# Performance work log

Measured on AMD Instinct MI355X. Metric: run time of the kernel, lower is better.

## Reference

```python
import jax, jax.numpy as jnp
import numpy as np

N = 20000      # atoms
E = 320000     # edges
F = 128        # node_size (hard-pinned by split(128) / expand to 384)
RBF = 20
RC = 5.0
ITERS = 3
NM = 64        # molecules in batch


def setup_inputs() -> dict:
    key = jax.random.key(0)
    ks = iter(jax.random.split(key, 64))
    def nrm(shape, scale=0.05):
        return jax.random.normal(next(ks), shape, dtype=jnp.float32) * scale
    inp = {}
    inp["z"] = jax.random.randint(next(ks), (N,), 0, 119)
    inp["graph"] = jax.random.randint(next(ks), (E, 2), 0, N)
    inp["edges_dist"] = jax.random.uniform(next(ks), (E,), minval=0.5, maxval=RC, dtype=jnp.float32)
    sense = jax.random.normal(next(ks), (E, 3), dtype=jnp.float32)
    inp["edges_sense"] = sense / jnp.linalg.norm(sense, axis=1, keepdims=True)
    inp["graph_idx"] = jnp.sort(jax.random.randint(next(ks), (N,), 0, NM))
    # parameters (stacked over ITERS message/update blocks)
    inp["emb"] = nrm((119, F), 1.0)
    inp["mw1"] = nrm((ITERS, F, F)); inp["mb1"] = nrm((ITERS, F))
    inp["mw2"] = nrm((ITERS, 3 * F, F)); inp["mb2"] = nrm((ITERS, 3 * F))
    inp["ew"] = nrm((ITERS, 3 * F, RBF)); inp["eb"] = nrm((ITERS, 3 * F))
    inp["uw"] = nrm((ITERS, F, F)); inp["vw"] = nrm((ITERS, F, F))
    inp["aw1"] = nrm((ITERS, F, 2 * F)); inp["ab1"] = nrm((ITERS, F))
    inp["aw2"] = nrm((ITERS, 3 * F, F)); inp["ab2"] = nrm((ITERS, 3 * F))
    inp["ow1"] = nrm((F, F)); inp["ob1"] = nrm((F,))
    inp["ow2"] = nrm((1, F)); inp["ob2"] = nrm((1,))
    return inp


def reference(z, graph, edges_dist, edges_sense, graph_idx,
              emb, mw1, mb1, mw2, mb2, ew, eb,
              uw, vw, aw1, ab1, aw2, ab2, ow1, ob1, ow2, ob2):
    src = graph[:, 0]   # scatter target (index_add index)
    dst = graph[:, 1]   # gather source (neighbour)
    s = emb[z]                                  # [N, F]
    v = jnp.zeros((N, 3, F), dtype=s.dtype)     # [N, 3, F]
    # edge-level precompute (same every iteration)
    n = jnp.arange(1, RBF + 1, dtype=jnp.float32)
    d = edges_dist[:, None]
    rbf = jnp.sin(n * jnp.pi * d / RC) / d                              # [E, RBF]
    cut = 0.5 * (jnp.cos(jnp.pi * edges_dist / RC) + 1.0) * (edges_dist < RC)  # [E]
    for i in range(ITERS):
        # --- Message block ---
        a = jax.nn.silu(s @ mw1[i].T + mb1[i]) @ mw2[i].T + mb2[i]      # [N, 3F]
        dist_rep = (rbf @ ew[i].T + eb[i]) * cut[:, None]               # [E, 3F]
        res = a[dst] * dist_rep                                         # [E, 3F]
        rv, rs, rd = res[:, :F], res[:, F:2 * F], res[:, 2 * F:]
        resv = v[dst] * rv[:, None, :] + edges_sense[:, :, None] * rd[:, None, :]  # [E,3,F]
        s = s + 2.0 * jax.ops.segment_sum(rs, src, num_segments=N)
        v = v + 2.0 * jax.ops.segment_sum(resv, src, num_segments=N)
        # --- Update block ---
        Uv = v @ uw[i].T                                                # [N,3,F]
        Vv = v @ vw[i].T
        h = jnp.concatenate([s, jnp.linalg.norm(Vv, axis=1)], axis=-1)  # [N, 2F]
        a2 = jax.nn.silu(h @ aw1[i].T + ab1[i]) @ aw2[i].T + ab2[i]     # [N, 3F]
        avv, asv, ass = a2[:, :F], a2[:, F:2 * F], a2[:, 2 * F:]
        s = s + ass + asv * jnp.sum(Uv * Vv, axis=1)
        v = v + avv[:, None, :] * Uv
    out = jax.nn.silu(s @ ow1.T + ob1) @ ow2.T + ob2                    # [N, 1]
    return jax.ops.segment_sum(out, graph_idx, num_segments=NM)         # [NM, 1]
```

## Files before the change

kernel.cpp:

```cpp
#include <hip/hip_runtime.h>
#include <math.h>

#define NN 20000
#define NE 320000
#define FD 128
#define RBFN 20
#define RC_ 5.0f
#define NITER 3
#define NMOL 64
#define F3 384
#define F2 256
#define PI_ 3.14159265358979323846f
#define KB 128
#define LPAD 8
#define SDS 392

typedef __attribute__((ext_vector_type(8))) short  bf16x8;
typedef __attribute__((ext_vector_type(4))) float  floatx4;
typedef unsigned short u16;
typedef unsigned int   u32;

__device__ __forceinline__ u16 f2b(float x) {
    union { float f; unsigned int u; } v; v.f = x;
    unsigned int u = v.u;
    return (u16)((u + 0x7fffu + ((u >> 16) & 1u)) >> 16);
}
__device__ __forceinline__ float b2f(u16 x) {
    union { unsigned int u; float f; } v; v.u = ((unsigned int)x) << 16;
    return v.f;
}

__global__ __launch_bounds__(256) void cvt_w_kernel(
    const float* s0, int n0, const float* s1, int n1, const float* s2, int n2,
    const float* s3, int n3, const float* s4, int n4, const float* s5, int n5,
    const float* s6, int n6, u16* __restrict__ dst)
{
    int idx = blockIdx.x * 256 + threadIdx.x;
    if (idx < n0) { dst[idx] = f2b(s0[idx]); return; } idx -= n0; dst += n0;
    if (idx < n1) { dst[idx] = f2b(s1[idx]); return; } idx -= n1; dst += n1;
    if (idx < n2) { dst[idx] = f2b(s2[idx]); return; } idx -= n2; dst += n2;
    if (idx < n3) { dst[idx] = f2b(s3[idx]); return; } idx -= n3; dst += n3;
    if (idx < n4) { dst[idx] = f2b(s4[idx]); return; } idx -= n4; dst += n4;
    if (idx < n5) { dst[idx] = f2b(s5[idx]); return; } idx -= n5; dst += n5;
    if (idx < n6) { dst[idx] = f2b(s6[idx]); }
}

__global__ __launch_bounds__(256) void cvt_ew_kernel(const float* __restrict__ ew,
    u16* __restrict__ ewb)
{
    int idx = blockIdx.x * 256 + threadIdx.x;
    if (idx >= NITER * F3 * 32) return;
    int k = idx & 31;
    int row = idx >> 5;
    ewb[idx] = (k < RBFN) ? f2b(ew[row * RBFN + k]) : (u16)0;
}

__global__ __launch_bounds__(256) void embed_kernel(const int* __restrict__ z,
    const float* __restrict__ emb, float* __restrict__ s, u16* __restrict__ sbf)
{
    int idx = blockIdx.x * 256 + threadIdx.x;
    if (idx >= NN * FD) return;
    int n = idx >> 7, f = idx & 127;
    float v = emb[z[n] * FD + f];
    s[idx] = v; sbf[idx] = f2b(v);
}

__global__ __launch_bounds__(256) void zero_f_kernel(float* __restrict__ p, int n)
{
    int idx = blockIdx.x * 256 + threadIdx.x;
    if (idx < n) p[idx] = 0.f;
}

__global__ __launch_bounds__(256) void zero_i_kernel(int* __restrict__ p, int n)
{
    int idx = blockIdx.x * 256 + threadIdx.x;
    if (idx < n) p[idx] = 0;
}

__global__ __launch_bounds__(256) void csr_count_kernel(const int* __restrict__ graph,
    int* __restrict__ cnt)
{
    int e = blockIdx.x * 256 + threadIdx.x;
    if (e >= NE) return;
    atomicAdd(&cnt[graph[2 * e]], 1);
}

__global__ __launch_bounds__(1024) void csr_scan_kernel(const int* __restrict__ cnt,
    int* __restrict__ row_ptr, int* __restrict__ cursor)
{
    __shared__ int sd[1024];
    int tid = threadIdx.x;
    const int chunk = (NN + 1023) / 1024;
    int start = tid * chunk;
    int end = start + chunk; if (end > NN) end = NN;
    int sum = 0;
    for (int j = start; j < end; j++) sum += cnt[j];
    sd[tid] = sum;
    __syncthreads();
    for (int off = 1; off < 1024; off <<= 1) {
        int v = 0;
        if (tid >= off) v = sd[tid - off];
        __syncthreads();
        if (tid >= off) sd[tid] += v;
        __syncthreads();
    }
    int run = (tid == 0) ? 0 : sd[tid - 1];
    for (int j = start; j < end; j++) {
        row_ptr[j] = run;
        cursor[j]  = run;
        run += cnt[j];
    }
    if (tid == 0) row_ptr[NN] = NE;
}

__global__ __launch_bounds__(256) void csr_scatter_kernel(const int* __restrict__ graph,
    int* __restrict__ cursor, int* __restrict__ edge_list)
{
    int e = blockIdx.x * 256 + threadIdx.x;
    if (e >= NE) return;
    int p = atomicAdd(&cursor[graph[2 * e]], 1);
    edge_list[p] = e;
}

__global__ __launch_bounds__(256) void edge_stream_kernel(
    const int* __restrict__ edge_list, const int* __restrict__ graph,
    const float* __restrict__ dist, const float* __restrict__ sense,
    u16* __restrict__ rbf_bf, float* __restrict__ cut_p,
    float* __restrict__ sense_p, int* __restrict__ dst_p)
{
    int j = blockIdx.x * 256 + threadIdx.x;
    if (j >= NE) return;
    int e = edge_list[j];
    float d = dist[e];
    float inv = 1.f / d;
    float base = PI_ * d / RC_;
    u16* rb = rbf_bf + (size_t)j * 32;
    #pragma unroll
    for (int k = 0; k < RBFN; k++)
        rb[k] = f2b(sinf((float)(k + 1) * base) * inv);
    #pragma unroll
    for (int k = RBFN; k < 32; k++) rb[k] = 0;
    cut_p[j] = 0.5f * (cosf(base) + 1.f) * (d < RC_ ? 1.f : 0.f);
    dst_p[j] = graph[2 * e + 1];
    sense_p[3 * j + 0] = sense[3 * e + 0];
    sense_p[3 * j + 1] = sense[3 * e + 1];
    sense_p[3 * j + 2] = sense[3 * e + 2];
}

template<bool SILU>
__global__ __launch_bounds__(256) void gemm_bf16(const u16* __restrict__ A,
    const u16* __restrict__ Wt, const float* __restrict__ bias,
    float* __restrict__ C, int M, int K, int Nc)
{
    __shared__ u16 As[64][KB + LPAD];
    __shared__ u16 Bs[64][KB + LPAD];
    const int bm = blockIdx.x * 64;
    const int bn = blockIdx.y * 64;
    const int tid = threadIdx.x;
    const int r = tid >> 2;
    const int q = tid & 3;
    const int wave = tid >> 6;
    const int lane = tid & 63;
    const int wm = (wave >> 1) * 32;
    const int wn = (wave & 1) * 32;
    const int quad = lane >> 4;
    const int lr = lane & 15;

    floatx4 acc[2][2];
    #pragma unroll
    for (int i = 0; i < 2; i++)
        #pragma unroll
        for (int j = 0; j < 2; j++)
            acc[i][j] = (floatx4)0.f;

    for (int ko = 0; ko < K; ko += KB) {
        {
            int gm = bm + r;
            u16* dA = &As[r][q * 32];
            if (gm < M) {
                const u16* ap = A + (size_t)gm * K + ko + q * 32;
                #pragma unroll
                for (int x = 0; x < 32; x += 8)
                    *(bf16x8*)&dA[x] = *(const bf16x8*)(ap + x);
            } else {
                #pragma unroll
                for (int x = 0; x < 32; x += 8)
                    *(bf16x8*)&dA[x] = (bf16x8)0;
            }
        }
        {
            int gn = bn + r;
            const u16* wp = Wt + (size_t)gn * K + ko + q * 32;
            u16* dB = &Bs[r][q * 32];
            #pragma unroll
            for (int x = 0; x < 32; x += 8)
                *(bf16x8*)&dB[x] = *(const bf16x8*)(wp + x);
        }
        __syncthreads();
        #pragma unroll
        for (int kk = 0; kk < KB; kk += 32) {
            bf16x8 a0 = *(const bf16x8*)&As[wm + lr     ][kk + quad * 8];
            bf16x8 a1 = *(const bf16x8*)&As[wm + 16 + lr][kk + quad * 8];
            bf16x8 b0 = *(const bf16x8*)&Bs[wn + lr     ][kk + quad * 8];
            bf16x8 b1 = *(const bf16x8*)&Bs[wn + 16 + lr][kk + quad * 8];
            acc[0][0] = __builtin_amdgcn_mfma_f32_16x16x32_bf16(a0, b0, acc[0][0], 0, 0, 0);
            acc[0][1] = __builtin_amdgcn_mfma_f32_16x16x32_bf16(a0, b1, acc[0][1], 0, 0, 0);
            acc[1][0] = __builtin_amdgcn_mfma_f32_16x16x32_bf16(a1, b0, acc[1][0], 0, 0, 0);
            acc[1][1] = __builtin_amdgcn_mfma_f32_16x16x32_bf16(a1, b1, acc[1][1], 0, 0, 0);
        }
        __syncthreads();
    }

    #pragma unroll
    for (int i = 0; i < 2; i++) {
        #pragma unroll
        for (int j = 0; j < 2; j++) {
            int gn = bn + wn + j * 16 + lr;
            float bb = bias ? bias[gn] : 0.f;
            #pragma unroll
            for (int rr = 0; rr < 4; rr++) {
                int gm = bm + wm + i * 16 + quad * 4 + rr;
                if (gm < M) {
                    float v = acc[i][j][rr] + bb;
                    if (SILU) v = v / (1.f + __expf(-v));
                    C[(size_t)gm * Nc + gn] = v;
                }
            }
        }
    }
}

template<int K1, bool PACK>
__global__ __launch_bounds__(256) void mlp_kernel(const u16* __restrict__ A,
    const u16* __restrict__ W1, const float* __restrict__ b1,
    const u16* __restrict__ W2, const float* __restrict__ b2,
    u16* __restrict__ Ob, int M)
{
    __shared__ u16 As[64][KB + LPAD];
    __shared__ u16 Ws[128][KB + LPAD];
    __shared__ u16 T[64][KB + LPAD];
    const int bm = blockIdx.x * 64;
    const int tid = threadIdx.x;
    const int wave = tid >> 6, lane = tid & 63;
    const int wm  = (wave >> 1) * 32;
    const int wn1 = (wave & 1) * 64;
    const int wn  = (wave & 1) * 32;
    const int quad = lane >> 4, lr = lane & 15;
    const int r = tid >> 2, q = tid & 3;

    floatx4 acc1[2][4];
    #pragma unroll
    for (int i = 0; i < 2; i++)
        #pragma unroll
        for (int j = 0; j < 4; j++) acc1[i][j] = (floatx4)0.f;

    for (int ko = 0; ko < K1; ko += KB) {
        {
            int gm = bm + r;
            u16* dA = &As[r][q * 32];
            if (gm < M) {
                const u16* ap = A + (size_t)gm * K1 + ko + q * 32;
                #pragma unroll
                for (int x = 0; x < 32; x += 8)
                    *(bf16x8*)&dA[x] = *(const bf16x8*)(ap + x);
            } else {
                #pragma unroll
                for (int x = 0; x < 32; x += 8)
                    *(bf16x8*)&dA[x] = (bf16x8)0;
            }
            #pragma unroll
            for (int h = 0; h < 2; h++) {
                int wr = r + h * 64;
                const u16* wp = W1 + (size_t)wr * K1 + ko + q * 32;
                u16* dW = &Ws[wr][q * 32];
                #pragma unroll
                for (int x = 0; x < 32; x += 8)
                    *(bf16x8*)&dW[x] = *(const bf16x8*)(wp + x);
            }
        }
        __syncthreads();
        #pragma unroll
        for (int kk = 0; kk < KB; kk += 32) {
            bf16x8 a0 = *(const bf16x8*)&As[wm + lr     ][kk + quad * 8];
            bf16x8 a1 = *(const bf16x8*)&As[wm + 16 + lr][kk + quad * 8];
            #pragma unroll
            for (int j = 0; j < 4; j++) {
                bf16x8 b = *(const bf16x8*)&Ws[wn1 + j * 16 + lr][kk + quad * 8];
                acc1[0][j] = __builtin_amdgcn_mfma_f32_16x16x32_bf16(a0, b, acc1[0][j], 0, 0, 0);
                acc1[1][j] = __builtin_amdgcn_mfma_f32_16x16x32_bf16(a1, b, acc1[1][j], 0, 0, 0);
            }
        }
        __syncthreads();
    }
    #pragma unroll
    for (int i = 0; i < 2; i++) {
        #pragma unroll
        for (int j = 0; j < 4; j++) {
            int col = wn1 + j * 16 + lr;
            float bb = b1[col];
            #pragma unroll
            for (int rr = 0; rr < 4; rr++) {
                int row = wm + i * 16 + quad * 4 + rr;
                float v = acc1[i][j][rr] + bb;
                v = v / (1.f + __expf(-v));
                T[row][col] = f2b(v);
            }
        }
    }
    __syncthreads();

    for (int c0 = 0; c0 < F3; c0 += 64) {
        {
            const u16* wp = W2 + (size_t)(c0 + r) * KB + q * 32;
            u16* dW = &Ws[r][q * 32];
            #pragma unroll
            for (int x = 0; x < 32; x += 8)
                *(bf16x8*)&dW[x] = *(const bf16x8*)(wp + x);
        }
        __syncthreads();
        floatx4 acc2[2][2];
        #pragma unroll
        for (int i = 0; i < 2; i++)
            #pragma unroll
            for (int j = 0; j < 2; j++) acc2[i][j] = (floatx4)0.f;
        #pragma unroll
        for (int kk = 0; kk < KB; kk += 32) {
            bf16x8 a0 = *(const bf16x8*)&T[wm + lr     ][kk + quad * 8];
            bf16x8 a1 = *(const bf16x8*)&T[wm + 16 + lr][kk + quad * 8];
            bf16x8 b0 = *(const bf16x8*)&Ws[wn + lr     ][kk + quad * 8];
            bf16x8 b1 = *(const bf16x8*)&Ws[wn + 16 + lr][kk + quad * 8];
            acc2[0][0] = __builtin_amdgcn_mfma_f32_16x16x32_bf16(a0, b0, acc2[0][0], 0, 0, 0);
            acc2[0][1] = __builtin_amdgcn_mfma_f32_16x16x32_bf16(a0, b1, acc2[0][1], 0, 0, 0);
            acc2[1][0] = __builtin_amdgcn_mfma_f32_16x16x32_bf16(a1, b0, acc2[1][0], 0, 0, 0);
            acc2[1][1] = __builtin_amdgcn_mfma_f32_16x16x32_bf16(a1, b1, acc2[1][1], 0, 0, 0);
        }
        #pragma unroll
        for (int i = 0; i < 2; i++) {
            #pragma unroll
            for (int j = 0; j < 2; j++) {
                int gn = c0 + wn + j * 16 + lr;
                float bb = b2[gn];
                #pragma unroll
                for (int rr = 0; rr < 4; rr++) {
                    int gm = bm + wm + i * 16 + quad * 4 + rr;
                    if (gm < M) {
                        u16 val = f2b(acc2[i][j][rr] + bb);
                        if (PACK) {
                            int off = (gn < 256) ? ((gn & 127) * 2 + (gn >> 7))
                                                 : (256 + (gn & 127));
                            Ob[(size_t)gm * F3 + off] = val;
                        } else {
                            Ob[(size_t)gm * F3 + gn] = val;
                        }
                    }
                }
            }
        }
        __syncthreads();
    }
}

__global__ __launch_bounds__(256) void gemm_uv(const u16* __restrict__ A,
    const u16* __restrict__ Wu, const u16* __restrict__ Wv,
    u16* __restrict__ U, u16* __restrict__ V, int M)
{
    __shared__ u16 As[64][KB + LPAD];
    __shared__ u16 Bu[64][KB + LPAD];
    __shared__ u16 Bv[64][KB + LPAD];
    const int bm = blockIdx.x * 64;
    const int bn = blockIdx.y * 64;
    const int tid = threadIdx.x;
    const int r = tid >> 2;
    const int q = tid & 3;
    const int wave = tid >> 6;
    const int lane = tid & 63;
    const int wm = (wave >> 1) * 32;
    const int wn = (wave & 1) * 32;
    const int quad = lane >> 4;
    const int lr = lane & 15;

    floatx4 au[2][2], av[2][2];
    #pragma unroll
    for (int i = 0; i < 2; i++)
        #pragma unroll
        for (int j = 0; j < 2; j++) { au[i][j] = (floatx4)0.f; av[i][j] = (floatx4)0.f; }

    {
        int gm = bm + r;
        u16* dA = &As[r][q * 32];
        if (gm < M) {
            const u16* ap = A + (size_t)gm * KB + q * 32;
            #pragma unroll
            for (int x = 0; x < 32; x += 8)
                *(bf16x8*)&dA[x] = *(const bf16x8*)(ap + x);
        } else {
            #pragma unroll
            for (int x = 0; x < 32; x += 8)
                *(bf16x8*)&dA[x] = (bf16x8)0;
        }
        int gn = bn + r;
        const u16* up = Wu + (size_t)gn * KB + q * 32;
        const u16* vp = Wv + (size_t)gn * KB + q * 32;
        u16* dU = &Bu[r][q * 32];
        u16* dV = &Bv[r][q * 32];
        #pragma unroll
        for (int x = 0; x < 32; x += 8) {
            *(bf16x8*)&dU[x] = *(const bf16x8*)(up + x);
            *(bf16x8*)&dV[x] = *(const bf16x8*)(vp + x);
        }
    }
    __syncthreads();
    #pragma unroll
    for (int kk = 0; kk < KB; kk += 32) {
        bf16x8 a0 = *(const bf16x8*)&As[wm + lr     ][kk + quad * 8];
        bf16x8 a1 = *(const bf16x8*)&As[wm + 16 + lr][kk + quad * 8];
        bf16x8 u0 = *(const bf16x8*)&Bu[wn + lr     ][kk + quad * 8];
        bf16x8 u1 = *(const bf16x8*)&Bu[wn + 16 + lr][kk + quad * 8];
        bf16x8 v0 = *(const bf16x8*)&Bv[wn + lr     ][kk + quad * 8];
        bf16x8 v1 = *(const bf16x8*)&Bv[wn + 16 + lr][kk + quad * 8];
        au[0][0] = __builtin_amdgcn_mfma_f32_16x16x32_bf16(a0, u0, au[0][0], 0, 0, 0);
        au[0][1] = __builtin_amdgcn_mfma_f32_16x16x32_bf16(a0, u1, au[0][1], 0, 0, 0);
        au[1][0] = __builtin_amdgcn_mfma_f32_16x16x32_bf16(a1, u0, au[1][0], 0, 0, 0);
        au[1][1] = __builtin_amdgcn_mfma_f32_16x16x32_bf16(a1, u1, au[1][1], 0, 0, 0);
        av[0][0] = __builtin_amdgcn_mfma_f32_16x16x32_bf16(a0, v0, av[0][0], 0, 0, 0);
        av[0][1] = __builtin_amdgcn_mfma_f32_16x16x32_bf16(a0, v1, av[0][1], 0, 0, 0);
        av[1][0] = __builtin_amdgcn_mfma_f32_16x16x32_bf16(a1, v0, av[1][0], 0, 0, 0);
        av[1][1] = __builtin_amdgcn_mfma_f32_16x16x32_bf16(a1, v1, av[1][1], 0, 0, 0);
    }
    #pragma unroll
    for (int i = 0; i < 2; i++) {
        #pragma unroll
        for (int j = 0; j < 2; j++) {
            int gn = bn + wn + j * 16 + lr;
            #pragma unroll
            for (int rr = 0; rr < 4; rr++) {
                int gm = bm + wm + i * 16 + quad * 4 + rr;
                if (gm < M) {
                    U[(size_t)gm * FD + gn] = f2b(au[i][j][rr]);
                    V[(size_t)gm * FD + gn] = f2b(av[i][j][rr]);
                }
            }
        }
    }
}

__global__ __launch_bounds__(256) void edge_mfma_kernel(
    const u16* __restrict__ rbf_bf, const float* __restrict__ cut_p,
    const float* __restrict__ sense_p, const int* __restrict__ dst_p,
    const u16* __restrict__ ewb, const float* __restrict__ eb,
    const u16* __restrict__ a_pk, const float* __restrict__ s_in,
    const float* __restrict__ v_in, const u16* __restrict__ v_pk,
    const int* __restrict__ row_ptr,
    float* __restrict__ s_out, u16* __restrict__ s_obf,
    float* __restrict__ v_out, u16* __restrict__ v_obf)
{
    __shared__ u16   sdrep[16 * SDS];
    __shared__ float scut[16];
    __shared__ float ssen[16][4];
    __shared__ int   sdst[16];
    __shared__ float red[4 * 128];

    const int n = blockIdx.x;
    const int tid = threadIdx.x;
    const int wave = tid >> 6;
    const int lane = tid & 63;
    const int quad = lane >> 4;
    const int lr = lane & 15;
    const int f = tid & 127;
    const int half = tid >> 7;

    int beg = row_ptr[n], end = row_ptr[n + 1];
    float accs = 0.f, accv0 = 0.f, accv1 = 0.f, accv2 = 0.f;

    for (int t0 = beg; t0 < end; t0 += 16) {
        int cnt = end - t0; if (cnt > 16) cnt = 16;
        __syncthreads();
        if (tid < 16) {
            scut[tid] = (tid < cnt) ? cut_p[t0 + tid] : 0.f;
            sdst[tid] = (tid < cnt) ? dst_p[t0 + tid] : 0;
        }
        if (tid >= 64 && tid < 64 + 3 * cnt) {
            int x = tid - 64;
            ssen[x / 3][x % 3] = sense_p[3 * t0 + x];
        }
        bf16x8 afrag;
        int ge = t0 + lr;
        if (ge < end) afrag = *(const bf16x8*)&rbf_bf[(size_t)ge * 32 + quad * 8];
        else          afrag = (bf16x8)0;
        floatx4 dacc[6];
        #pragma unroll
        for (int nt = 0; nt < 6; nt++) {
            int nrow = (wave * 6 + nt) * 16 + lr;
            bf16x8 bfrag = *(const bf16x8*)&ewb[(size_t)nrow * 32 + quad * 8];
            dacc[nt] = __builtin_amdgcn_mfma_f32_16x16x32_bf16(afrag, bfrag, (floatx4)0.f, 0, 0, 0);
        }
        __syncthreads();
        #pragma unroll
        for (int nt = 0; nt < 6; nt++) {
            int ncol = (wave * 6 + nt) * 16 + lr;
            float ebn = eb[ncol];
            #pragma unroll
            for (int rr = 0; rr < 4; rr++) {
                int e = quad * 4 + rr;
                sdrep[e * SDS + ncol] = f2b((dacc[nt][rr] + ebn) * scut[e]);
            }
        }
        __syncthreads();
        int nh = cnt - half * 8; if (nh > 8) nh = 8;
        for (int k = 0; k < nh; k++) {
            int e = half * 8 + k;
            int dst = sdst[e];
            const u16* sr = &sdrep[e * SDS];
            float drv = b2f(sr[f]);
            float drs = b2f(sr[FD + f]);
            float drd = b2f(sr[2 * FD + f]);
            const u16* ar = a_pk + (size_t)dst * F3;
            u32 ap = *(const u32*)(ar + f * 2);
            float rv = b2f((u16)(ap & 0xffff)) * drv;
            float rs = b2f((u16)(ap >> 16))    * drs;
            float rd = b2f(ar[256 + f])        * drd;
            accs += rs;
            const u16* vr = v_pk + (size_t)dst * F3;
            u32 vp = *(const u32*)(vr + f * 2);
            accv0 += b2f((u16)(vp & 0xffff)) * rv + ssen[e][0] * rd;
            accv1 += b2f((u16)(vp >> 16))    * rv + ssen[e][1] * rd;
            accv2 += b2f(vr[256 + f])        * rv + ssen[e][2] * rd;
        }
    }
    __syncthreads();
    if (half == 1) {
        red[f] = accs; red[128 + f] = accv0; red[256 + f] = accv1; red[384 + f] = accv2;
    }
    __syncthreads();
    if (half == 0) {
        accs  += red[f];       accv0 += red[128 + f];
        accv1 += red[256 + f]; accv2 += red[384 + f];
        int nb = n * FD + f;
        float so = s_in[nb] + 2.f * accs;
        s_out[nb] = so; s_obf[nb] = f2b(so);
        int vb = n * F3 + f;
        float w0 = v_in[vb]           + 2.f * accv0;
        float w1 = v_in[vb + FD]      + 2.f * accv1;
        float w2 = v_in[vb + 2 * FD]  + 2.f * accv2;
        v_out[vb]          = w0; v_obf[vb]          = f2b(w0);
        v_out[vb + FD]     = w1; v_obf[vb + FD]     = f2b(w1);
        v_out[vb + 2 * FD] = w2; v_obf[vb + 2 * FD] = f2b(w2);
    }
}

__global__ __launch_bounds__(256) void build_h_kernel(const u16* __restrict__ sbf,
    const u16* __restrict__ Vv, u16* __restrict__ h)
{
    int idx = blockIdx.x * 256 + threadIdx.x;
    if (idx >= NN * FD) return;
    int n = idx >> 7, f = idx & 127;
    h[n * F2 + f] = sbf[idx];
    float x0 = b2f(Vv[n * F3 + f]);
    float x1 = b2f(Vv[n * F3 + FD + f]);
    float x2 = b2f(Vv[n * F3 + 2 * FD + f]);
    h[n * F2 + FD + f] = f2b(sqrtf(x0 * x0 + x1 * x1 + x2 * x2));
}

__global__ __launch_bounds__(256) void update_kernel(const float* __restrict__ s_mid,
    const float* __restrict__ v_mid, const u16* __restrict__ a2,
    const u16* __restrict__ Uv, const u16* __restrict__ Vv,
    float* __restrict__ s_out, u16* __restrict__ s_obf,
    float* __restrict__ v_out, u16* __restrict__ v_pk)
{
    int idx = blockIdx.x * 256 + threadIdx.x;
    if (idx >= NN * FD) return;
    int n = idx >> 7, f = idx & 127;
    int vb = n * F3 + f;
    float u0 = b2f(Uv[vb]), u1 = b2f(Uv[vb + FD]), u2 = b2f(Uv[vb + 2 * FD]);
    float w0 = b2f(Vv[vb]), w1 = b2f(Vv[vb + FD]), w2 = b2f(Vv[vb + 2 * FD]);
    float dot = u0 * w0 + u1 * w1 + u2 * w2;
    float avv = b2f(a2[n * F3 + f]);
    float asv = b2f(a2[n * F3 + FD + f]);
    float ass = b2f(a2[n * F3 + 2 * FD + f]);
    float so = s_mid[idx] + ass + asv * dot;
    s_out[idx] = so; s_obf[idx] = f2b(so);
    float y0 = v_mid[vb]          + avv * u0;
    float y1 = v_mid[vb + FD]     + avv * u1;
    float y2 = v_mid[vb + 2 * FD] + avv * u2;
    v_out[vb]          = y0;
    v_out[vb + FD]     = y1;
    v_out[vb + 2 * FD] = y2;
    u16* vp = v_pk + (size_t)n * F3;
    *(u32*)(vp + f * 2) = (u32)f2b(y0) | ((u32)f2b(y1) << 16);
    vp[256 + f] = f2b(y2);
}

__global__ __launch_bounds__(256) void node_out_kernel(const float* __restrict__ t,
    const float* __restrict__ ow2, const float* __restrict__ ob2,
    float* __restrict__ nodeval)
{
    int gt = blockIdx.x * 256 + threadIdx.x;
    int n = gt >> 6;
    int lane = threadIdx.x & 63;
    if (n >= NN) return;
    float v = t[n * FD + lane] * ow2[lane] + t[n * FD + 64 + lane] * ow2[64 + lane];
    #pragma unroll
    for (int off = 32; off > 0; off >>= 1) v += __shfl_down(v, off);
    if (lane == 0) nodeval[n] = v + ob2[0];
}

__global__ __launch_bounds__(1024) void mol_reduce_kernel(const float* __restrict__ nodeval,
    const int* __restrict__ gidx, float* __restrict__ out)
{
    __shared__ float mol[NMOL];
    int tid = threadIdx.x;
    if (tid < NMOL) mol[tid] = 0.f;
    __syncthreads();
    int cur = -1; float acc = 0.f;
    for (int x = tid; x < NN; x += 1024) {
        int g = gidx[x];
        float v = nodeval[x];
        if (g != cur) {
            if (cur >= 0) atomicAdd(&mol[cur], acc);
            cur = g; acc = v;
        } else acc += v;
    }
    if (cur >= 0) atomicAdd(&mol[cur], acc);
    __syncthreads();
    if (tid < NMOL) out[tid] = mol[tid];
}

extern "C" void kernel_launch(void* const* d_in, const int* in_sizes, int n_in,
                              void* d_out, int out_size, void* d_ws, size_t ws_size,
                              hipStream_t stream)
{
    const int*   z     = (const int*)d_in[0];
    const int*   graph = (const int*)d_in[1];
    const float* dist  = (const float*)d_in[2];
    const float* sense = (const float*)d_in[3];
    const int*   gidx  = (const int*)d_in[4];
    const float* emb   = (const float*)d_in[5];
    const float* mw1   = (const float*)d_in[6];
    const float* mb1   = (const float*)d_in[7];
    const float* mw2   = (const float*)d_in[8];
    const float* mb2   = (const float*)d_in[9];
    const float* ew    = (const float*)d_in[10];
    const float* eb    = (const float*)d_in[11];
    const float* uw    = (const float*)d_in[12];
    const float* vw    = (const float*)d_in[13];
    const float* aw1   = (const float*)d_in[14];
    const float* ab1   = (const float*)d_in[15];
    const float* aw2   = (const float*)d_in[16];
    const float* ab2   = (const float*)d_in[17];
    const float* ow1   = (const float*)d_in[18];
    const float* ob1   = (const float*)d_in[19];
    const float* ow2   = (const float*)d_in[20];
    const float* ob2   = (const float*)d_in[21];
    float* out = (float*)d_out;

    float* W = (float*)d_ws;
    float* s_a    = W; W += (size_t)NN * FD;
    float* s_b    = W; W += (size_t)NN * FD;
    float* v_a    = W; W += (size_t)NN * F3;
    float* v_b    = W; W += (size_t)NN * F3;
    float* cut_p  = W; W += (size_t)NE;
    float* sns_p  = W; W += (size_t)NE * 3;
    float* nodeval= W; W += (size_t)NN;
    u16* U = (u16*)W;
    u16* sbf_a = U; U += (size_t)NN * FD;
    u16* sbf_b = U; U += (size_t)NN * FD;
    u16* vbf_b = U; U += (size_t)NN * F3;
    u16* a_pk  = U; U += (size_t)NN * F3;
    u16* v_pk  = U; U += (size_t)NN * F3;
    u16* h_bf  = U; U += (size_t)NN * F2;
    u16* a2_bf = U; U += (size_t)NN * F3;
    u16* Uv_bf = U; U += (size_t)NN * F3;
    u16* Vv_bf = U; U += (size_t)NN * F3;
    u16* rbf_bf= U; U += (size_t)NE * 32;
    u16* ewb   = U; U += (size_t)NITER * F3 * 32;
    u16* wb    = U; U += 557056;
    int* ip = (int*)U;
    int* row_ptr   = ip; ip += NN + 1;
    int* cnt       = ip; ip += NN;
    int* cursor    = ip; ip += NN;
    int* edge_list = ip; ip += NE;
    int* dst_p     = ip; ip += NE;
    float* tfin = s_b;

    u16* wb_mw1 = wb;
    u16* wb_mw2 = wb + 49152;
    u16* wb_uw  = wb + 196608;
    u16* wb_vw  = wb + 245760;
    u16* wb_aw1 = wb + 294912;
    u16* wb_aw2 = wb + 393216;
    u16* wb_ow1 = wb + 540672;
    const int WTOT = 557056;

    const int TB = 256;
    dim3 b256(TB);

    cvt_w_kernel<<<dim3((WTOT + TB - 1) / TB), b256, 0, stream>>>(
        mw1, 49152, mw2, 147456, uw, 49152, vw, 49152, aw1, 98304, aw2, 147456,
        ow1, 16384, wb);
    cvt_ew_kernel<<<dim3((NITER * F3 * 32 + TB - 1) / TB), b256, 0, stream>>>(ew, ewb);
    embed_kernel<<<dim3((NN * FD + TB - 1) / TB), b256, 0, stream>>>(z, emb, s_a, sbf_a);
    zero_f_kernel<<<dim3((NN * F3 + TB - 1) / TB), b256, 0, stream>>>(v_a, NN * F3);
    zero_i_kernel<<<dim3((NN * F3 / 2 + TB - 1) / TB), b256, 0, stream>>>((int*)v_pk, NN * F3 / 2);
    zero_i_kernel<<<dim3((NN + TB - 1) / TB), b256, 0, stream>>>(cnt, NN);
    csr_count_kernel<<<dim3((NE + TB - 1) / TB), b256, 0, stream>>>(graph, cnt);
    csr_scan_kernel<<<dim3(1), dim3(1024), 0, stream>>>(cnt, row_ptr, cursor);
    csr_scatter_kernel<<<dim3((NE + TB - 1) / TB), b256, 0, stream>>>(graph, cursor, edge_list);
    edge_stream_kernel<<<dim3((NE + TB - 1) / TB), b256, 0, stream>>>(
        edge_list, graph, dist, sense, rbf_bf, cut_p, sns_p, dst_p);

    dim3 gM((NN + 63) / 64);
    dim3 gN2((NN + 63) / 64, FD / 64);
    dim3 gV2((3 * NN + 63) / 64, FD / 64);

    for (int i = 0; i < NITER; i++) {
        mlp_kernel<128, true><<<gM, b256, 0, stream>>>(sbf_a,
            wb_mw1 + (size_t)i * FD * FD, mb1 + (size_t)i * FD,
            wb_mw2 + (size_t)i * F3 * FD, mb2 + (size_t)i * F3, a_pk, NN);
        edge_mfma_kernel<<<dim3(NN), b256, 0, stream>>>(
            rbf_bf, cut_p, sns_p, dst_p,
            ewb + (size_t)i * F3 * 32, eb + (size_t)i * F3,
            a_pk, s_a, v_a, v_pk, row_ptr, s_b, sbf_b, v_b, vbf_b);
        gemm_uv<<<gV2, b256, 0, stream>>>(vbf_b, wb_uw + (size_t)i * FD * FD,
            wb_vw + (size_t)i * FD * FD, Uv_bf, Vv_bf, 3 * NN);
        build_h_kernel<<<dim3((NN * FD + TB - 1) / TB), b256, 0, stream>>>(sbf_b, Vv_bf, h_bf);
        mlp_kernel<256, false><<<gM, b256, 0, stream>>>(h_bf,
            wb_aw1 + (size_t)i * FD * F2, ab1 + (size_t)i * FD,
            wb_aw2 + (size_t)i * F3 * FD, ab2 + (size_t)i * F3, a2_bf, NN);
        update_kernel<<<dim3((NN * FD + TB - 1) / TB), b256, 0, stream>>>(
            s_b, v_b, a2_bf, Uv_bf, Vv_bf, s_a, sbf_a, v_a, v_pk);
    }

    gemm_bf16<true><<<gN2, b256, 0, stream>>>(sbf_a, wb_ow1, ob1, tfin, NN, FD, FD);
    node_out_kernel<<<dim3((NN * 64 + TB - 1) / TB), b256, 0, stream>>>(tfin, ow2, ob2, nodeval);
    mol_reduce_kernel<<<dim3(1), dim3(1024), 0, stream>>>(nodeval, gidx, out);
}
```

Measured before the change: 948.9 us.

## Interleave message and vector features per node for wider gathers in edge kernel

The separate packed message buffer and packed vector buffer are merged into one per-node 768-element interleaved row, so each edge reads a (rv, rs, v0, v1) quad with one 8-byte load and a (rd, v2) pair with one 4-byte load, where it used to issue several scattered loads across two buffers. The MLP epilogue and the update kernel now write into this shared layout, and the edge-filter LDS tile is stored in a matching packed order so each edge needs two LDS reads instead of three. The edge-filter weight fragments and bias are also hoisted into registers once per block rather than reloaded every 16-edge tile. The merge adds register pressure and makes the producers write strided, interleaved rows.

```diff
diff --git a/kernel.cpp b/kernel.cpp
--- a/kernel.cpp
+++ b/kernel.cpp
@@ -346,9 +346,9 @@
                     if (gm < M) {
                         u16 val = f2b(acc2[i][j][rr] + bb);
                         if (PACK) {
-                            int off = (gn < 256) ? ((gn & 127) * 2 + (gn >> 7))
-                                                 : (256 + (gn & 127));
-                            Ob[(size_t)gm * F3 + off] = val;
+                            int fc = gn & 127;
+                            int off = (gn < 256) ? (fc * 4 + (gn >> 7)) : (512 + fc * 2);
+                            Ob[(size_t)gm * 768 + off] = val;
                         } else {
                             Ob[(size_t)gm * F3 + gn] = val;
                         }
@@ -448,8 +448,8 @@
     const u16* __restrict__ rbf_bf, const float* __restrict__ cut_p,
     const float* __restrict__ sense_p, const int* __restrict__ dst_p,
     const u16* __restrict__ ewb, const float* __restrict__ eb,
-    const u16* __restrict__ a_pk, const float* __restrict__ s_in,
-    const float* __restrict__ v_in, const u16* __restrict__ v_pk,
+    const u16* __restrict__ apv, const float* __restrict__ s_in,
+    const float* __restrict__ v_in,
     const int* __restrict__ row_ptr,
     float* __restrict__ s_out, u16* __restrict__ s_obf,
     float* __restrict__ v_out, u16* __restrict__ v_obf)
@@ -469,6 +469,15 @@
     const int f = tid & 127;
     const int half = tid >> 7;
 
+    bf16x8 bfrag[6];
+    float  ebv[6];
+    #pragma unroll
+    for (int nt = 0; nt < 6; nt++) {
+        int nrow = (wave * 6 + nt) * 16 + lr;
+        bfrag[nt] = *(const bf16x8*)&ewb[(size_t)nrow * 32 + quad * 8];
+        ebv[nt]   = eb[nrow];
+    }
+
     int beg = row_ptr[n], end = row_ptr[n + 1];
     float accs = 0.f, accv0 = 0.f, accv1 = 0.f, accv2 = 0.f;
 
@@ -489,42 +498,40 @@
         else          afrag = (bf16x8)0;
         floatx4 dacc[6];
         #pragma unroll
-        for (int nt = 0; nt < 6; nt++) {
-            int nrow = (wave * 6 + nt) * 16 + lr;
-            bf16x8 bfrag = *(const bf16x8*)&ewb[(size_t)nrow * 32 + quad * 8];
-            dacc[nt] = __builtin_amdgcn_mfma_f32_16x16x32_bf16(afrag, bfrag, (floatx4)0.f, 0, 0, 0);
-        }
+        for (int nt = 0; nt < 6; nt++)
+            dacc[nt] = __builtin_amdgcn_mfma_f32_16x16x32_bf16(afrag, bfrag[nt], (floatx4)0.f, 0, 0, 0);
         __syncthreads();
         #pragma unroll
         for (int nt = 0; nt < 6; nt++) {
             int ncol = (wave * 6 + nt) * 16 + lr;
-            float ebn = eb[ncol];
+            int fc = ncol & 127;
+            int off = (ncol < 256) ? (fc * 2 + (ncol >> 7)) : (256 + fc);
             #pragma unroll
             for (int rr = 0; rr < 4; rr++) {
                 int e = quad * 4 + rr;
-                sdrep[e * SDS + ncol] = f2b((dacc[nt][rr] + ebn) * scut[e]);
+                sdrep[e * SDS + off] = f2b((dacc[nt][rr] + ebv[nt]) * scut[e]);
             }
         }
         __syncthreads();
         int nh = cnt - half * 8; if (nh > 8) nh = 8;
+        int base = half * 8;
         for (int k = 0; k < nh; k++) {
-            int e = half * 8 + k;
+            int e = base + k;
             int dst = sdst[e];
-            const u16* sr = &sdrep[e * SDS];
-            float drv = b2f(sr[f]);
-            float drs = b2f(sr[FD + f]);
-            float drd = b2f(sr[2 * FD + f]);
-            const u16* ar = a_pk + (size_t)dst * F3;
-            u32 ap = *(const u32*)(ar + f * 2);
-            float rv = b2f((u16)(ap & 0xffff)) * drv;
-            float rs = b2f((u16)(ap >> 16))    * drs;
-            float rd = b2f(ar[256 + f])        * drd;
+            u32 drp = *(const u32*)&sdrep[e * SDS + f * 2];
+            float drv = b2f((u16)(drp & 0xffff));
+            float drs = b2f((u16)(drp >> 16));
+            float drd = b2f(sdrep[e * SDS + 256 + f]);
+            const u16* row = apv + (size_t)dst * 768;
+            uint2 qv = *(const uint2*)(row + f * 4);
+            u32  p2 = *(const u32*)(row + 512 + f * 2);
+            float rv = b2f((u16)(qv.x & 0xffff)) * drv;
+            float rs = b2f((u16)(qv.x >> 16))    * drs;
+            float rd = b2f((u16)(p2 & 0xffff))   * drd;
             accs += rs;
-            const u16* vr = v_pk + (size_t)dst * F3;
-            u32 vp = *(const u32*)(vr + f * 2);
-            accv0 += b2f((u16)(vp & 0xffff)) * rv + ssen[e][0] * rd;
-            accv1 += b2f((u16)(vp >> 16))    * rv + ssen[e][1] * rd;
-            accv2 += b2f(vr[256 + f])        * rv + ssen[e][2] * rd;
+            accv0 += b2f((u16)(qv.y & 0xffff)) * rv + ssen[e][0] * rd;
+            accv1 += b2f((u16)(qv.y >> 16))    * rv + ssen[e][1] * rd;
+            accv2 += b2f((u16)(p2 >> 16))      * rv + ssen[e][2] * rd;
         }
     }
     __syncthreads();
@@ -565,7 +572,7 @@
     const float* __restrict__ v_mid, const u16* __restrict__ a2,
     const u16* __restrict__ Uv, const u16* __restrict__ Vv,
     float* __restrict__ s_out, u16* __restrict__ s_obf,
-    float* __restrict__ v_out, u16* __restrict__ v_pk)
+    float* __restrict__ v_out, u16* __restrict__ apv)
 {
     int idx = blockIdx.x * 256 + threadIdx.x;
     if (idx >= NN * FD) return;
@@ -585,9 +592,9 @@
     v_out[vb]          = y0;
     v_out[vb + FD]     = y1;
     v_out[vb + 2 * FD] = y2;
-    u16* vp = v_pk + (size_t)n * F3;
-    *(u32*)(vp + f * 2) = (u32)f2b(y0) | ((u32)f2b(y1) << 16);
-    vp[256 + f] = f2b(y2);
+    u16* vp = apv + (size_t)n * 768;
+    *(u32*)(vp + f * 4 + 2) = (u32)f2b(y0) | ((u32)f2b(y1) << 16);
+    vp[512 + f * 2 + 1] = f2b(y2);
 }
 
 __global__ __launch_bounds__(256) void node_out_kernel(const float* __restrict__ t,
@@ -665,8 +672,7 @@
     u16* sbf_a = U; U += (size_t)NN * FD;
     u16* sbf_b = U; U += (size_t)NN * FD;
     u16* vbf_b = U; U += (size_t)NN * F3;
-    u16* a_pk  = U; U += (size_t)NN * F3;
-    u16* v_pk  = U; U += (size_t)NN * F3;
+    u16* apv   = U; U += (size_t)NN * 768;
     u16* h_bf  = U; U += (size_t)NN * F2;
     u16* a2_bf = U; U += (size_t)NN * F3;
     u16* Uv_bf = U; U += (size_t)NN * F3;
@@ -700,7 +706,7 @@
     cvt_ew_kernel<<<dim3((NITER * F3 * 32 + TB - 1) / TB), b256, 0, stream>>>(ew, ewb);
     embed_kernel<<<dim3((NN * FD + TB - 1) / TB), b256, 0, stream>>>(z, emb, s_a, sbf_a);
     zero_f_kernel<<<dim3((NN * F3 + TB - 1) / TB), b256, 0, stream>>>(v_a, NN * F3);
-    zero_i_kernel<<<dim3((NN * F3 / 2 + TB - 1) / TB), b256, 0, stream>>>((int*)v_pk, NN * F3 / 2);
+    zero_i_kernel<<<dim3((NN * 384 + TB - 1) / TB), b256, 0, stream>>>((int*)apv, NN * 384);
     zero_i_kernel<<<dim3((NN + TB - 1) / TB), b256, 0, stream>>>(cnt, NN);
     csr_count_kernel<<<dim3((NE + TB - 1) / TB), b256, 0, stream>>>(graph, cnt);
     csr_scan_kernel<<<dim3(1), dim3(1024), 0, stream>>>(cnt, row_ptr, cursor);
@@ -715,11 +721,11 @@
     for (int i = 0; i < NITER; i++) {
         mlp_kernel<128, true><<<gM, b256, 0, stream>>>(sbf_a,
             wb_mw1 + (size_t)i * FD * FD, mb1 + (size_t)i * FD,
-            wb_mw2 + (size_t)i * F3 * FD, mb2 + (size_t)i * F3, a_pk, NN);
+            wb_mw2 + (size_t)i * F3 * FD, mb2 + (size_t)i * F3, apv, NN);
         edge_mfma_kernel<<<dim3(NN), b256, 0, stream>>>(
             rbf_bf, cut_p, sns_p, dst_p,
             ewb + (size_t)i * F3 * 32, eb + (size_t)i * F3,
-            a_pk, s_a, v_a, v_pk, row_ptr, s_b, sbf_b, v_b, vbf_b);
+            apv, s_a, v_a, row_ptr, s_b, sbf_b, v_b, vbf_b);
         gemm_uv<<<gV2, b256, 0, stream>>>(vbf_b, wb_uw + (size_t)i * FD * FD,
             wb_vw + (size_t)i * FD * FD, Uv_bf, Vv_bf, 3 * NN);
         build_h_kernel<<<dim3((NN * FD + TB - 1) / TB), b256, 0, stream>>>(sbf_b, Vv_bf, h_bf);
@@ -727,7 +733,7 @@
             wb_aw1 + (size_t)i * FD * F2, ab1 + (size_t)i * FD,
             wb_aw2 + (size_t)i * F3 * FD, ab2 + (size_t)i * F3, a2_bf, NN);
         update_kernel<<<dim3((NN * FD + TB - 1) / TB), b256, 0, stream>>>(
-            s_b, v_b, a2_bf, Uv_bf, Vv_bf, s_a, sbf_a, v_a, v_pk);
+            s_b, v_b, a2_bf, Uv_bf, Vv_bf, s_a, sbf_a, v_a, apv);
     }
 
     gemm_bf16<true><<<gN2, b256, 0, stream>>>(sbf_a, wb_ow1, ob1, tfin, NN, FD, FD);
```

New measurement: 988.9 us. 1.04x slower.

## Widen edge kernel to 512 threads, hoist edge weights, pack dist_rep in LDS

Applied to the files above, without the earlier changes.

The per-node edge kernel now runs 512 threads (8 waves), so each wave computes 3 MFMA column tiles instead of 6. The edge-weight fragments and biases are loaded once into registers before the edge loop instead of being reloaded for every 16-edge chunk. The dist_rep tile in shared memory is stored in the same interleaved layout as a_pk, so v/s pairs are read with one 32-bit load. The four thread groups each handle 4 of the 16 edges in a chunk and are reduced through a larger shared buffer. This adds parallelism for the gather-heavy loop, at the cost of idle threads on low-degree nodes and extra reduction work.

```diff
diff --git a/kernel.cpp b/kernel.cpp
--- a/kernel.cpp
+++ b/kernel.cpp
@@ -346,8 +346,8 @@
                     if (gm < M) {
                         u16 val = f2b(acc2[i][j][rr] + bb);
                         if (PACK) {
-                            int off = (gn < 256) ? ((gn & 127) * 2 + (gn >> 7))
-                                                 : (256 + (gn & 127));
+                            int fc = gn & 127;
+                            int off = (gn < 256) ? (fc * 2 + (gn >> 7)) : (256 + fc);
                             Ob[(size_t)gm * F3 + off] = val;
                         } else {
                             Ob[(size_t)gm * F3 + gn] = val;
@@ -444,7 +444,7 @@
     }
 }
 
-__global__ __launch_bounds__(256) void edge_mfma_kernel(
+__global__ __launch_bounds__(512) void edge_mfma_kernel(
     const u16* __restrict__ rbf_bf, const float* __restrict__ cut_p,
     const float* __restrict__ sense_p, const int* __restrict__ dst_p,
     const u16* __restrict__ ewb, const float* __restrict__ eb,
@@ -458,7 +458,7 @@
     __shared__ float scut[16];
     __shared__ float ssen[16][4];
     __shared__ int   sdst[16];
-    __shared__ float red[4 * 128];
+    __shared__ float red[3 * 512];
 
     const int n = blockIdx.x;
     const int tid = threadIdx.x;
@@ -467,7 +467,16 @@
     const int quad = lane >> 4;
     const int lr = lane & 15;
     const int f = tid & 127;
-    const int half = tid >> 7;
+    const int qt = tid >> 7;
+
+    bf16x8 bfrag[3];
+    float  ebv[3];
+    #pragma unroll
+    for (int nt = 0; nt < 3; nt++) {
+        int nrow = (wave * 3 + nt) * 16 + lr;
+        bfrag[nt] = *(const bf16x8*)&ewb[(size_t)nrow * 32 + quad * 8];
+        ebv[nt]   = eb[nrow];
+    }
 
     int beg = row_ptr[n], end = row_ptr[n + 1];
     float accs = 0.f, accv0 = 0.f, accv1 = 0.f, accv2 = 0.f;
@@ -487,33 +496,32 @@
         int ge = t0 + lr;
         if (ge < end) afrag = *(const bf16x8*)&rbf_bf[(size_t)ge * 32 + quad * 8];
         else          afrag = (bf16x8)0;
-        floatx4 dacc[6];
-        #pragma unroll
-        for (int nt = 0; nt < 6; nt++) {
-            int nrow = (wave * 6 + nt) * 16 + lr;
-            bf16x8 bfrag = *(const bf16x8*)&ewb[(size_t)nrow * 32 + quad * 8];
-            dacc[nt] = __builtin_amdgcn_mfma_f32_16x16x32_bf16(afrag, bfrag, (floatx4)0.f, 0, 0, 0);
-        }
-        __syncthreads();
-        #pragma unroll
-        for (int nt = 0; nt < 6; nt++) {
-            int ncol = (wave * 6 + nt) * 16 + lr;
-            float ebn = eb[ncol];
+        floatx4 dacc[3];
+        #pragma unroll
+        for (int nt = 0; nt < 3; nt++)
+            dacc[nt] = __builtin_amdgcn_mfma_f32_16x16x32_bf16(afrag, bfrag[nt], (floatx4)0.f, 0, 0, 0);
+        __syncthreads();
+        #pragma unroll
+        for (int nt = 0; nt < 3; nt++) {
+            int ncol = (wave * 3 + nt) * 16 + lr;
+            int fc = ncol & 127;
+            int off = (ncol < 256) ? (fc * 2 + (ncol >> 7)) : (256 + fc);
             #pragma unroll
             for (int rr = 0; rr < 4; rr++) {
                 int e = quad * 4 + rr;
-                sdrep[e * SDS + ncol] = f2b((dacc[nt][rr] + ebn) * scut[e]);
-            }
-        }
-        __syncthreads();
-        int nh = cnt - half * 8; if (nh > 8) nh = 8;
+                sdrep[e * SDS + off] = f2b((dacc[nt][rr] + ebv[nt]) * scut[e]);
+            }
+        }
+        __syncthreads();
+        int base = qt * 4;
+        int nh = cnt - base; if (nh > 4) nh = 4;
         for (int k = 0; k < nh; k++) {
-            int e = half * 8 + k;
+            int e = base + k;
             int dst = sdst[e];
-            const u16* sr = &sdrep[e * SDS];
-            float drv = b2f(sr[f]);
-            float drs = b2f(sr[FD + f]);
-            float drd = b2f(sr[2 * FD + f]);
+            u32 drp = *(const u32*)&sdrep[e * SDS + f * 2];
+            float drv = b2f((u16)(drp & 0xffff));
+            float drs = b2f((u16)(drp >> 16));
+            float drd = b2f(sdrep[e * SDS + 256 + f]);
             const u16* ar = a_pk + (size_t)dst * F3;
             u32 ap = *(const u32*)(ar + f * 2);
             float rv = b2f((u16)(ap & 0xffff)) * drv;
@@ -528,13 +536,18 @@
         }
     }
     __syncthreads();
-    if (half == 1) {
-        red[f] = accs; red[128 + f] = accv0; red[256 + f] = accv1; red[384 + f] = accv2;
+    if (qt > 0) {
+        float* rp = &red[(qt - 1) * 512];
+        rp[f] = accs; rp[128 + f] = accv0; rp[256 + f] = accv1; rp[384 + f] = accv2;
     }
     __syncthreads();
-    if (half == 0) {
-        accs  += red[f];       accv0 += red[128 + f];
-        accv1 += red[256 + f]; accv2 += red[384 + f];
+    if (qt == 0) {
+        #pragma unroll
+        for (int qq = 0; qq < 3; qq++) {
+            const float* rp = &red[qq * 512];
+            accs  += rp[f];       accv0 += rp[128 + f];
+            accv1 += rp[256 + f]; accv2 += rp[384 + f];
+        }
         int nb = n * FD + f;
         float so = s_in[nb] + 2.f * accs;
         s_out[nb] = so; s_obf[nb] = f2b(so);
@@ -716,7 +729,7 @@
         mlp_kernel<128, true><<<gM, b256, 0, stream>>>(sbf_a,
             wb_mw1 + (size_t)i * FD * FD, mb1 + (size_t)i * FD,
             wb_mw2 + (size_t)i * F3 * FD, mb2 + (size_t)i * F3, a_pk, NN);
-        edge_mfma_kernel<<<dim3(NN), b256, 0, stream>>>(
+        edge_mfma_kernel<<<dim3(NN), dim3(512), 0, stream>>>(
             rbf_bf, cut_p, sns_p, dst_p,
             ewb + (size_t)i * F3 * 32, eb + (size_t)i * F3,
             a_pk, s_a, v_a, v_pk, row_ptr, s_b, sbf_b, v_b, vbf_b);
```

Result: slower. 1.034 ms (+8.9%).

## Fuse vector-norm h construction into update MLP and hoist edge weight fragments

Applied to the files above, without the earlier changes.

Replaces the separate build_h kernel and the generic two-layer MLP with a dedicated kernel that builds the [s, |Vv|] input tile directly in shared memory while loading, removing the intermediate h buffer write and read plus one launch. The edge kernel now loads its RBF weight fragments and biases into registers once per block instead of every 16-edge tile. It also stores the dist_rep tile in the interleaved packed layout so the v/s components are read with one 32-bit LDS load. This adds register pressure in the edge kernel and recomputes the norm per M-tile, which is not redundant here since each N tile covers all columns.

```diff
diff --git a/kernel.cpp b/kernel.cpp
--- a/kernel.cpp
+++ b/kernel.cpp
@@ -346,13 +346,154 @@
                     if (gm < M) {
                         u16 val = f2b(acc2[i][j][rr] + bb);
                         if (PACK) {
-                            int off = (gn < 256) ? ((gn & 127) * 2 + (gn >> 7))
-                                                 : (256 + (gn & 127));
+                            int fc = gn & 127;
+                            int off = (gn < 256) ? (fc * 2 + (gn >> 7)) : (256 + fc);
                             Ob[(size_t)gm * F3 + off] = val;
                         } else {
                             Ob[(size_t)gm * F3 + gn] = val;
                         }
                     }
+                }
+            }
+        }
+        __syncthreads();
+    }
+}
+
+__global__ __launch_bounds__(256) void amlp_kernel(const u16* __restrict__ sbf,
+    const u16* __restrict__ Vv,
+    const u16* __restrict__ W1, const float* __restrict__ b1,
+    const u16* __restrict__ W2, const float* __restrict__ b2,
+    u16* __restrict__ Ob, int M)
+{
+    __shared__ u16 As[64][KB + LPAD];
+    __shared__ u16 Ws[128][KB + LPAD];
+    __shared__ u16 T[64][KB + LPAD];
+    const int bm = blockIdx.x * 64;
+    const int tid = threadIdx.x;
+    const int wave = tid >> 6, lane = tid & 63;
+    const int wm  = (wave >> 1) * 32;
+    const int wn1 = (wave & 1) * 64;
+    const int wn  = (wave & 1) * 32;
+    const int quad = lane >> 4, lr = lane & 15;
+    const int r = tid >> 2, q = tid & 3;
+
+    floatx4 acc1[2][4];
+    #pragma unroll
+    for (int i = 0; i < 2; i++)
+        #pragma unroll
+        for (int j = 0; j < 4; j++) acc1[i][j] = (floatx4)0.f;
+
+    for (int ko = 0; ko < F2; ko += KB) {
+        {
+            int gm = bm + r;
+            u16* dA = &As[r][q * 32];
+            if (gm < M) {
+                if (ko == 0) {
+                    const u16* ap = sbf + (size_t)gm * FD + q * 32;
+                    #pragma unroll
+                    for (int x = 0; x < 32; x += 8)
+                        *(bf16x8*)&dA[x] = *(const bf16x8*)(ap + x);
+                } else {
+                    const u16* vr = Vv + (size_t)gm * F3 + q * 32;
+                    #pragma unroll
+                    for (int x = 0; x < 32; x += 8) {
+                        bf16x8 c0 = *(const bf16x8*)(vr + x);
+                        bf16x8 c1 = *(const bf16x8*)(vr + FD + x);
+                        bf16x8 c2 = *(const bf16x8*)(vr + 2 * FD + x);
+                        bf16x8 o;
+                        #pragma unroll
+                        for (int t = 0; t < 8; t++) {
+                            float a = b2f((u16)c0[t]);
+                            float b = b2f((u16)c1[t]);
+                            float c = b2f((u16)c2[t]);
+                            o[t] = (short)f2b(sqrtf(a * a + b * b + c * c));
+                        }
+                        *(bf16x8*)&dA[x] = o;
+                    }
+                }
+            } else {
+                #pragma unroll
+                for (int x = 0; x < 32; x += 8)
+                    *(bf16x8*)&dA[x] = (bf16x8)0;
+            }
+            #pragma unroll
+            for (int h = 0; h < 2; h++) {
+                int wr = r + h * 64;
+                const u16* wp = W1 + (size_t)wr * F2 + ko + q * 32;
+                u16* dW = &Ws[wr][q * 32];
+                #pragma unroll
+                for (int x = 0; x < 32; x += 8)
+                    *(bf16x8*)&dW[x] = *(const bf16x8*)(wp + x);
+            }
+        }
+        __syncthreads();
+        #pragma unroll
+        for (int kk = 0; kk < KB; kk += 32) {
+            bf16x8 a0 = *(const bf16x8*)&As[wm + lr     ][kk + quad * 8];
+            bf16x8 a1 = *(const bf16x8*)&As[wm + 16 + lr][kk + quad * 8];
+            #pragma unroll
+            for (int j = 0; j < 4; j++) {
+                bf16x8 b = *(const bf16x8*)&Ws[wn1 + j * 16 + lr][kk + quad * 8];
+                acc1[0][j] = __builtin_amdgcn_mfma_f32_16x16x32_bf16(a0, b, acc1[0][j], 0, 0, 0);
+                acc1[1][j] = __builtin_amdgcn_mfma_f32_16x16x32_bf16(a1, b, acc1[1][j], 0, 0, 0);
+            }
+        }
+        __syncthreads();
+    }
+    #pragma unroll
+    for (int i = 0; i < 2; i++) {
+        #pragma unroll
+        for (int j = 0; j < 4; j++) {
+            int col = wn1 + j * 16 + lr;
+            float bb = b1[col];
+            #pragma unroll
+            for (int rr = 0; rr < 4; rr++) {
+                int row = wm + i * 16 + quad * 4 + rr;
+                float v = acc1[i][j][rr] + bb;
+                v = v / (1.f + __expf(-v));
+                T[row][col] = f2b(v);
+            }
+        }
+    }
+    __syncthreads();
+
+    for (int c0 = 0; c0 < F3; c0 += 64) {
+        {
+            const u16* wp = W2 + (size_t)(c0 + r) * KB + q * 32;
+            u16* dW = &Ws[r][q * 32];
+            #pragma unroll
+            for (int x = 0; x < 32; x += 8)
+                *(bf16x8*)&dW[x] = *(const bf16x8*)(wp + x);
+        }
+        __syncthreads();
+        floatx4 acc2[2][2];
+        #pragma unroll
+        for (int i = 0; i < 2; i++)
+            #pragma unroll
+            for (int j = 0; j < 2; j++) acc2[i][j] = (floatx4)0.f;
+        #pragma unroll
+        for (int kk = 0; kk < KB; kk += 32) {
+            bf16x8 a0 = *(const bf16x8*)&T[wm + lr     ][kk + quad * 8];
+            bf16x8 a1 = *(const bf16x8*)&T[wm + 16 + lr][kk + quad * 8];
+            bf16x8 b0 = *(const bf16x8*)&Ws[wn + lr     ][kk + quad * 8];
+            bf16x8 b1 = *(const bf16x8*)&Ws[wn + 16 + lr][kk + quad * 8];
+            acc2[0][0] = __builtin_amdgcn_mfma_f32_16x16x32_bf16(a0, b0, acc2[0][0], 0, 0, 0);
+            acc2[0][1] = __builtin_amdgcn_mfma_f32_16x16x32_bf16(a0, b1, acc2[0][1], 0, 0, 0);
+            acc2[1][0] = __builtin_amdgcn_mfma_f32_16x16x32_bf16(a1, b0, acc2[1][0], 0, 0, 0);
+            acc2[1][1] = __builtin_amdgcn_mfma_f32_16x16x32_bf16(a1, b1, acc2[1][1], 0, 0, 0);
+        }
+        #pragma unroll
+        for (int i = 0; i < 2; i++) {
+            #pragma unroll
+            for (int j = 0; j < 2; j++) {
+                int gn = c0 + wn + j * 16 + lr;
+                float bb = b2[gn];
+                #pragma unroll
+                for (int rr = 0; rr < 4; rr++) {
+                    int gm = bm + wm + i * 16 + quad * 4 + rr;
+                    if (gm < M)
+                        Ob[(size_t)gm * F3 + gn] = f2b(acc2[i][j][rr] + bb);
                 }
             }
         }
@@ -469,6 +610,15 @@
     const int f = tid & 127;
     const int half = tid >> 7;
 
+    bf16x8 bfrag[6];
+    float  ebv[6];
+    #pragma unroll
+    for (int nt = 0; nt < 6; nt++) {
+        int nrow = (wave * 6 + nt) * 16 + lr;
+        bfrag[nt] = *(const bf16x8*)&ewb[(size_t)nrow * 32 + quad * 8];
+        ebv[nt]   = eb[nrow];
+    }
+
     int beg = row_ptr[n], end = row_ptr[n + 1];
     float accs = 0.f, accv0 = 0.f, accv1 = 0.f, accv2 = 0.f;
 
@@ -489,31 +639,30 @@
         else          afrag = (bf16x8)0;
         floatx4 dacc[6];
         #pragma unroll
-        for (int nt = 0; nt < 6; nt++) {
-            int nrow = (wave * 6 + nt) * 16 + lr;
-            bf16x8 bfrag = *(const bf16x8*)&ewb[(size_t)nrow * 32 + quad * 8];
-            dacc[nt] = __builtin_amdgcn_mfma_f32_16x16x32_bf16(afrag, bfrag, (floatx4)0.f, 0, 0, 0);
-        }
+        for (int nt = 0; nt < 6; nt++)
+            dacc[nt] = __builtin_amdgcn_mfma_f32_16x16x32_bf16(afrag, bfrag[nt], (floatx4)0.f, 0, 0, 0);
         __syncthreads();
         #pragma unroll
         for (int nt = 0; nt < 6; nt++) {
             int ncol = (wave * 6 + nt) * 16 + lr;
-            float ebn = eb[ncol];
+            int fc = ncol & 127;
+            int off = (ncol < 256) ? (fc * 2 + (ncol >> 7)) : (256 + fc);
             #pragma unroll
             for (int rr = 0; rr < 4; rr++) {
                 int e = quad * 4 + rr;
-                sdrep[e * SDS + ncol] = f2b((dacc[nt][rr] + ebn) * scut[e]);
+                sdrep[e * SDS + off] = f2b((dacc[nt][rr] + ebv[nt]) * scut[e]);
             }
         }
         __syncthreads();
         int nh = cnt - half * 8; if (nh > 8) nh = 8;
+        int base = half * 8;
         for (int k = 0; k < nh; k++) {
-            int e = half * 8 + k;
+            int e = base + k;
             int dst = sdst[e];
-            const u16* sr = &sdrep[e * SDS];
-            float drv = b2f(sr[f]);
-            float drs = b2f(sr[FD + f]);
-            float drd = b2f(sr[2 * FD + f]);
+            u32 drp = *(const u32*)&sdrep[e * SDS + f * 2];
+            float drv = b2f((u16)(drp & 0xffff));
+            float drs = b2f((u16)(drp >> 16));
+            float drd = b2f(sdrep[e * SDS + 256 + f]);
             const u16* ar = a_pk + (size_t)dst * F3;
             u32 ap = *(const u32*)(ar + f * 2);
             float rv = b2f((u16)(ap & 0xffff)) * drv;
@@ -546,19 +695,6 @@
         v_out[vb + FD]     = w1; v_obf[vb + FD]     = f2b(w1);
         v_out[vb + 2 * FD] = w2; v_obf[vb + 2 * FD] = f2b(w2);
     }
-}
-
-__global__ __launch_bounds__(256) void build_h_kernel(const u16* __restrict__ sbf,
-    const u16* __restrict__ Vv, u16* __restrict__ h)
-{
-    int idx = blockIdx.x * 256 + threadIdx.x;
-    if (idx >= NN * FD) return;
-    int n = idx >> 7, f = idx & 127;
-    h[n * F2 + f] = sbf[idx];
-    float x0 = b2f(Vv[n * F3 + f]);
-    float x1 = b2f(Vv[n * F3 + FD + f]);
-    float x2 = b2f(Vv[n * F3 + 2 * FD + f]);
-    h[n * F2 + FD + f] = f2b(sqrtf(x0 * x0 + x1 * x1 + x2 * x2));
 }
 
 __global__ __launch_bounds__(256) void update_kernel(const float* __restrict__ s_mid,
@@ -667,7 +803,6 @@
     u16* vbf_b = U; U += (size_t)NN * F3;
     u16* a_pk  = U; U += (size_t)NN * F3;
     u16* v_pk  = U; U += (size_t)NN * F3;
-    u16* h_bf  = U; U += (size_t)NN * F2;
     u16* a2_bf = U; U += (size_t)NN * F3;
     u16* Uv_bf = U; U += (size_t)NN * F3;
     u16* Vv_bf = U; U += (size_t)NN * F3;
@@ -722,8 +857,7 @@
             a_pk, s_a, v_a, v_pk, row_ptr, s_b, sbf_b, v_b, vbf_b);
         gemm_uv<<<gV2, b256, 0, stream>>>(vbf_b, wb_uw + (size_t)i * FD * FD,
             wb_vw + (size_t)i * FD * FD, Uv_bf, Vv_bf, 3 * NN);
-        build_h_kernel<<<dim3((NN * FD + TB - 1) / TB), b256, 0, stream>>>(sbf_b, Vv_bf, h_bf);
-        mlp_kernel<256, false><<<gM, b256, 0, stream>>>(h_bf,
+        amlp_kernel<<<gM, b256, 0, stream>>>(sbf_b, Vv_bf,
             wb_aw1 + (size_t)i * FD * F2, ab1 + (size_t)i * FD,
             wb_aw2 + (size_t)i * F3 * FD, ab2 + (size_t)i * F3, a2_bf, NN);
         update_kernel<<<dim3((NN * FD + TB - 1) / TB), b256, 0, stream>>>(
```

Result: no change. 962.6 us (+1.4%).
